# Optimization experiments

Measured on AMD Instinct MI355X. Metric: run time of the kernel, lower is better.

The kernel has to match this reference:

```python
import jax, jax.numpy as jnp
import numpy as np

NUM_CLASSES = 80
TOPK = 1000
CONF_THRESH = 0.05
NMS_THRESH = 0.6
IMG = 1280.0  # input image H = W
LEVEL_N = [230400, 57600, 14400, 3600, 900]  # (1280/stride)^2 * 9 anchors, strides 8..128


def _make_boxes(k, n):
    kc, kw = jax.random.split(k)
    cxcy = jax.random.uniform(kc, (n, 2), jnp.float32, 0.0, IMG)
    wh = jax.random.uniform(kw, (n, 2), jnp.float32, 8.0, 256.0)
    x1y1 = jnp.clip(cxcy - 0.5 * wh, 0.0, IMG)
    x2y2 = jnp.clip(cxcy + 0.5 * wh, 0.0, IMG)
    return jnp.concatenate([x1y1, x2y2], axis=-1)  # [n,4] xyxy pixel coords


def setup_inputs() -> dict:
    key = jax.random.key(0)
    keys = jax.random.split(key, 10)
    inp = {}
    for i, n in enumerate(LEVEL_N):
        inp[f"cls{i}"] = jax.random.normal(keys[i], (n, NUM_CLASSES), jnp.float32) - 2.0
        inp[f"box{i}"] = _make_boxes(keys[5 + i], n)
    return inp


def _level_topk(cls_l, box_l):
    # cls_l: [N, C] logits, box_l: [N, 4]
    n = cls_l.shape[0]
    scores = jax.nn.sigmoid(cls_l).reshape(-1)           # [N*C]
    k = min(TOPK, n)
    top_scores, top_idx = jax.lax.top_k(scores, k)       # fused sort/topk per level
    labels = top_idx % NUM_CLASSES
    anchor = top_idx // NUM_CLASSES
    boxes = box_l[anchor]                                # irregular gather
    valid = top_scores > CONF_THRESH
    return top_scores, labels, boxes, valid


def _pairwise_iou(b):
    # b: [M,4] xyxy
    area = jnp.maximum(b[:, 2] - b[:, 0], 0.0) * jnp.maximum(b[:, 3] - b[:, 1], 0.0)
    lt = jnp.maximum(b[:, None, :2], b[None, :, :2])
    rb = jnp.minimum(b[:, None, 2:], b[None, :, 2:])
    wh = jnp.maximum(rb - lt, 0.0)
    inter = wh[..., 0] * wh[..., 1]
    return inter / (area[:, None] + area[None, :] - inter + 1e-9)


def _greedy_nms(boxes, scores, labels, valid):
    # class-aware greedy NMS via per-class coordinate offset trick
    m = scores.shape[0]
    s = jnp.where(valid, scores, 0.0)
    order = jnp.argsort(-s)
    boxes = boxes[order]
    s = s[order]
    labels = labels[order]
    valid = valid[order]
    offset = labels.astype(boxes.dtype)[:, None] * (IMG + 1.0)
    ious = _pairwise_iou(boxes + offset)                 # [M,M]
    idx = jnp.arange(m)

    def body(i, keep):
        sup = keep[i] & (ious[i] > NMS_THRESH) & (idx > i)
        return keep & ~sup

    keep = jax.lax.fori_loop(0, m, body, valid)
    return boxes, s, labels, keep


def reference(cls0, cls1, cls2, cls3, cls4, box0, box1, box2, box3, box4):
    cls_preds = [cls0, cls1, cls2, cls3, cls4]
    box_preds = [box0, box1, box2, box3, box4]
    parts = [_level_topk(c, b) for c, b in zip(cls_preds, box_preds)]
    scores = jnp.concatenate([p[0] for p in parts])
    labels = jnp.concatenate([p[1] for p in parts])
    boxes = jnp.concatenate([p[2] for p in parts])
    valid = jnp.concatenate([p[3] for p in parts])
    boxes, scores, labels, keep = _greedy_nms(boxes, scores, labels, valid)
    keepf = keep.astype(boxes.dtype)
    bboxes = jnp.clip(boxes / IMG, 0.0, 1.0) * keepf[:, None]  # normalize like inference_single_image
    scores = scores * keepf
    return bboxes, scores, labels, keep
```

## Files before the change

### kernel.cpp

```cpp
#include <hip/hip_runtime.h>
#include <cmath>

typedef unsigned int u32;
typedef unsigned long long u64;

#define NLEV 5
#define M_TOT 4900
#define NWORDS 77
#define CSTRIDE 80
#define PAD_M 4928
#define NBLK 2999
#define LDSQ 2048
#define NSH 32
#define SHCAP 2048
#define OVCAP 16384
#define NREG 33
#define LVST (NSH*SHCAP + OVCAP)
#define TIE_CAP 4096
#define NBLK_CMAT 3003
#define HBINS 4096
#define UCAP 128

__constant__ int   c_KLVL[5] = {1000,1000,1000,1000,900};
__constant__ int   c_LOFF[5] = {0,1000,2000,3000,4000};
__constant__ int   c_N4[5]   = {4608000,1152000,288000,72000,18000};
__constant__ int   c_BB[6]   = {0,2250,2813,2954,2990,2999};
__constant__ float c_THR[5]  = {1.0f,0.65f,0.30f,-0.15f,-0.60f};

constexpr size_t OFF_CNT   = 0;
constexpr size_t OFF_OCNT  = 768;
constexpr size_t OFF_KEPT  = 1024;
constexpr size_t OFF_HPRED = 2048;
constexpr size_t OFF_C0    = 2816;
constexpr size_t OFF_KK    = 2848;
constexpr size_t OFF_EMITC = 2880;
constexpr size_t OFF_TIEC  = 2912;
constexpr size_t OFF_GHIST = 4096;
constexpr size_t ZERO_BYTES= OFF_GHIST + (size_t)NLEV*HBINS*4;
constexpr size_t OFF_TIEB  = ZERO_BYTES;
constexpr size_t OFF_CAND  = OFF_TIEB + (size_t)NLEV*TIE_CAP*8;
constexpr size_t OFF_KEY   = OFF_CAND + (size_t)NLEV*LVST*8;
constexpr size_t OFF_RAWB  = OFF_KEY   + (size_t)PAD_M*8;
constexpr size_t OFF_OFFB  = OFF_RAWB  + (size_t)PAD_M*16;
constexpr size_t OFF_LAB   = OFF_OFFB  + (size_t)PAD_M*16;
constexpr size_t OFF_SVAL  = OFF_LAB   + (size_t)PAD_M*4;
constexpr size_t OFF_VALID = OFF_SVAL  + (size_t)PAD_M*4;
constexpr size_t OFF_SRAWB = OFF_VALID + (size_t)PAD_M*4;
constexpr size_t OFF_SOFFB = OFF_SRAWB + (size_t)PAD_M*16;
constexpr size_t OFF_SLAB  = OFF_SOFFB + (size_t)PAD_M*16;
constexpr size_t OFF_SSVAL = OFF_SLAB  + (size_t)PAD_M*4;
constexpr size_t OFF_SVALID= OFF_SSVAL + (size_t)PAD_M*4;
constexpr size_t OFF_CMAT  = (OFF_SVALID + (size_t)PAD_M*4 + 255) & ~(size_t)255;

__device__ __forceinline__ u32 okey(u32 u){
  return (u & 0x80000000u) ? ~u : (u | 0x80000000u);
}

__device__ __forceinline__ u32 qbin(u32 bits, float T){
  float x = __uint_as_float(bits);
  int b = (int)((x - T)*800.0f);
  return (u32)max(0, min(HBINS-1, b));
}

__device__ __forceinline__ u32 lane_prior(u64 mask){
  return __builtin_amdgcn_mbcnt_hi((u32)(mask>>32),
         __builtin_amdgcn_mbcnt_lo((u32)mask, 0u));
}

__device__ __forceinline__ u32 wave_alloc(u32* ctr, bool take){
  u64 mask = __ballot(take);
  if (mask==0ull) return 0xFFFFFFFFu;
  u32 prior = lane_prior(mask);
  u32 total = (u32)__popcll(mask);
  int leader = __ffsll((unsigned long long)mask) - 1;
  u32 base = 0;
  if (take && prior==0u) base = atomicAdd(ctr, total);
  base = __shfl(base, leader, 64);
  return take ? (base + prior) : 0xFFFFFFFFu;
}

__device__ __forceinline__ const u32* region_ptr(u32* cand, int l, int r){
  return cand + ((size_t)l*LVST + ((r<NSH)?(size_t)r*SHCAP:(size_t)NSH*SHCAP))*2u;
}

__global__ void __launch_bounds__(256)
k_collect(const float* __restrict__ a0, const float* __restrict__ a1,
          const float* __restrict__ a2, const float* __restrict__ a3,
          const float* __restrict__ a4,
          u32* __restrict__ cnt, u32* __restrict__ ocnt, u32* __restrict__ cand)
{
  const int b = blockIdx.x;
  const int l = (b<c_BB[1])?0:(b<c_BB[2])?1:(b<c_BB[3])?2:(b<c_BB[4])?3:4;
  const float* __restrict__ p = (l==0)?a0:(l==1)?a1:(l==2)?a2:(l==3)?a3:a4;
  const float T = c_THR[l];
  const int n4l = c_N4[l];
  const int lb  = b - c_BB[l];
  const int shard = lb & (NSH-1);
  const int base4 = lb*2048 + (int)threadIdx.x;

  __shared__ u32 lcnt, gbase;
  __shared__ u32 lbitsA[LDSQ];
  __shared__ u32 lidxA[LDSQ];
  if (threadIdx.x==0) lcnt=0u;
  __syncthreads();

  float4 xs[8];
#pragma unroll
  for (int u=0;u<8;u++){
    int q = base4 + u*256;
    int qc = (q < n4l) ? q : (n4l-1);
    xs[u] = *(const float4*)(p + (size_t)qc*4u);
  }
  u32* cdS = cand + ((size_t)l*LVST + (size_t)shard*SHCAP)*2u;
  u32* cdO = cand + ((size_t)l*LVST + (size_t)NSH*SHCAP)*2u;
#pragma unroll
  for (int u=0;u<8;u++){
    int q = base4 + u*256;
    if (q < n4l){
      float v[4]={xs[u].x,xs[u].y,xs[u].z,xs[u].w};
#pragma unroll
      for (int i=0;i<4;i++){
        if (v[i] > T){
          u32 s = atomicAdd(&lcnt,1u);
          u32 bits = __float_as_uint(v[i]);
          u32 idx  = (u32)(q*4+i);
          if (s < LDSQ){ lbitsA[s]=bits; lidxA[s]=idx; }
          else {
            u32 pp = atomicAdd(&ocnt[l],1u);
            if (pp < OVCAP){ u32* d=cdO+(size_t)pp*2u; d[0]=bits; d[1]=idx; }
          }
        }
      }
    }
  }
  __syncthreads();
  if (threadIdx.x==0){
    u32 m = min(lcnt,(u32)LDSQ);
    gbase = (m>0u) ? atomicAdd(&cnt[l*NSH+shard],m) : 0xFFFFFFFFu;
  }
  __syncthreads();
  u32 m = min(lcnt,(u32)LDSQ);
  for (u32 i=threadIdx.x;i<m;i+=256u){
    u32 pp = gbase + i;
    if (pp < SHCAP){ u32* d=cdS+(size_t)pp*2u; d[0]=lbitsA[i]; d[1]=lidxA[i]; }
    else {
      u32 q = atomicAdd(&ocnt[l],1u);
      if (q < OVCAP){ u32* d=cdO+(size_t)q*2u; d[0]=lbitsA[i]; d[1]=lidxA[i]; }
    }
  }
}

__global__ void __launch_bounds__(256)
k_hist(const u32* __restrict__ cnt, const u32* __restrict__ ocnt,
       u32* __restrict__ cand, u32* __restrict__ ghist)
{
  const int l = blockIdx.x / NREG;
  const int r = blockIdx.x % NREG;
  const u32 len = (r<NSH) ? min(cnt[l*NSH+r],(u32)SHCAP) : min(ocnt[l],(u32)OVCAP);
  __shared__ u32 lh[HBINS];
  for (u32 i=threadIdx.x;i<(u32)HBINS;i+=256u) lh[i]=0u;
  __syncthreads();
  if (len){
    const u32* cdR = region_ptr(cand,l,r);
    const float Tl = c_THR[l];
    for (u32 i=threadIdx.x;i<len;i+=256u)
      atomicAdd(&lh[qbin(cdR[2*(size_t)i],Tl)],1u);
  }
  __syncthreads();
  u32* gh = ghist + (u32)l*HBINS;
  for (u32 i=threadIdx.x;i<(u32)HBINS;i+=256u){
    u32 v=lh[i];
    if (v) atomicAdd(&gh[i],v);
  }
}

__global__ void __launch_bounds__(1024)
k_cut(u32* __restrict__ cnt, u32* __restrict__ ocnt, u32* __restrict__ cand,
      u32* __restrict__ ghist,
      const float* __restrict__ a0, const float* __restrict__ a1,
      const float* __restrict__ a2, const float* __restrict__ a3,
      const float* __restrict__ a4,
      u32* __restrict__ c0A, u32* __restrict__ kkA)
{
  const int l = blockIdx.x;
  const int k = c_KLVL[l];
  const float Tl = c_THR[l];
  const float* __restrict__ p = (l==0)?a0:(l==1)?a1:(l==2)?a2:(l==3)?a3:a4;
  u32* cdO = cand + ((size_t)l*LVST + (size_t)NSH*SHCAP)*2u;
  u32* gh = ghist + (u32)l*HBINS;

  __shared__ u32 rlen[NREG];
  __shared__ u32 count_s, sufw[16];
  __shared__ u32 c0_s, kk_s;
  const u32 tid=threadIdx.x, lane=tid&63u, wave=tid>>6;
  if (tid<NSH) rlen[tid]=min(cnt[l*NSH+tid],(u32)SHCAP);
  if (tid==NSH) rlen[NSH]=min(ocnt[l],(u32)OVCAP);
  if (tid==0){ c0_s=0u; kk_s=(u32)k; }
  __syncthreads();
  if (tid==0){ u32 c=0; for(int r=0;r<NREG;r++) c+=rlen[r]; count_s=c; }
  __syncthreads();
  u32 count = count_s;

  if (count < (u32)k){
    const int nElem = c_N4[l]*4;
    float Tprev = Tl;
    u32 oc0 = rlen[NSH];
    for (int r=1; r<=7 && count<(u32)k; r++){
      float Tn = (r<7) ? (Tl - 1.5f*(float)r) : -3.0e38f;
      for (u32 i=tid; i<(u32)nElem; i+=1024u){
        float x = p[i];
        if (x>Tn && x<=Tprev){
          u32 pp = atomicAdd(&ocnt[l],1u);
          if (pp<OVCAP){ u32* d=cdO+(size_t)pp*2u; d[0]=__float_as_uint(x); d[1]=i; }
        }
      }
      __syncthreads();
      if (tid==0){
        rlen[NSH]=min(atomicAdd(&ocnt[l],0u),(u32)OVCAP);
        u32 c=0; for(int rr=0;rr<NREG;rr++) c+=rlen[rr]; count_s=c;
      }
      __syncthreads();
      count = count_s;
      Tprev = Tn;
    }
    if (tid==0 && rlen[NSH]>oc0) atomicAdd(&gh[0], rlen[NSH]-oc0);
    __syncthreads();
  }

  if (count > (u32)k){
    u32 base = tid*4u;
    u32 hb[4]; u32 ls=0u;
#pragma unroll
    for (int b2_=0;b2_<4;b2_++){ u32 h=gh[base+(u32)b2_]; hb[b2_]=h; ls+=h; }
    u32 x = ls;
#pragma unroll
    for (int off=1; off<64; off<<=1){
      u32 y = __shfl_down(x, off, 64);
      if (lane + (u32)off < 64u) x += y;
    }
    if (lane==0u) sufw[wave]=x;
    __syncthreads();
    u32 wsuf=0u;
    for (u32 w=wave+1u;w<16u;w++) wsuf += sufw[w];
    u32 suffix_after = wsuf + (x - ls);
    if (suffix_after < (u32)k && (u32)k <= suffix_after + ls){
      u32 run = suffix_after;
      for (int b2_=3;b2_>=0;b2_--){
        u32 h = hb[b2_];
        run += h;
        if (run >= (u32)k){ c0_s = base+(u32)b2_; kk_s = (u32)k - (run - h); break; }
      }
    }
    __syncthreads();
  }
  if (tid==0){ c0A[l]=c0_s; kkA[l]=kk_s; }
}

__device__ __forceinline__ void emit_record(int l, int slot, u32 lbits, u32 idx,
    const float4* __restrict__ boxp, u64* keyA, float4* rawbA, float4* offbA,
    u32* labA, float* svalA, u32* validA)
{
#pragma clang fp contract(off)
  float x = __uint_as_float(lbits);
  float s = (float)(1.0 / (1.0 + exp(-(double)x)));
  u32 valid = (s > 0.05f) ? 1u : 0u;
  u32 label = idx % 80u;
  u32 anchor = idx / 80u;
  float4 bx = boxp[anchor];
  float off = (float)label * 1281.0f;
  float4 ob;
  ob.x = bx.x + off; ob.y = bx.y + off; ob.z = bx.z + off; ob.w = bx.w + off;
  u32 pos = ((u32)l << 25) | idx;
  u32 khi = valid ? okey(lbits) : 0u;
  int g = c_LOFF[l] + slot;
  keyA[g]  = ((u64)khi << 32) | (u64)(u32)(~pos);
  rawbA[g] = bx; offbA[g] = ob; labA[g] = label;
  svalA[g] = valid ? s : 0.0f; validA[g] = valid;
}

__device__ __forceinline__ void emit_dummy(int l, int slot,
    u64* keyA, float4* rawbA, float4* offbA, u32* labA, float* svalA, u32* validA)
{
  u32 pos = ((u32)l<<25) | (0x1FFFFFFu - (u32)slot);
  int g = c_LOFF[l]+slot;
  float4 z; z.x=z.y=z.z=z.w=0.0f;
  keyA[g]=(u64)(u32)(~pos);
  rawbA[g]=z; offbA[g]=z; labA[g]=0u; svalA[g]=0.0f; validA[g]=0u;
}

__global__ void __launch_bounds__(256)
k_emit(const u32* __restrict__ cnt, const u32* __restrict__ ocnt,
       u32* __restrict__ cand,
       const u32* __restrict__ c0A,
       u32* __restrict__ emitc, u32* __restrict__ tiec, u32* __restrict__ tieb,
       const float4* b0, const float4* b1, const float4* b2,
       const float4* b3, const float4* b4,
       u64* keyA, float4* rawbA, float4* offbA,
       u32* labA, float* svalA, u32* validA)
{
  const int l = blockIdx.x / NREG;
  const int r = blockIdx.x % NREG;
  const u32 len = (r<NSH) ? min(cnt[l*NSH+r],(u32)SHCAP) : min(ocnt[l],(u32)OVCAP);
  if (len==0u) return;
  const float4* boxp = (l==0)?b0:(l==1)?b1:(l==2)?b2:(l==3)?b3:b4;
  const u32* cdR = region_ptr(cand,l,r);
  const float Tl = c_THR[l];
  const u32 c0 = c0A[l];
  const int k = c_KLVL[l];
  u32* tbL = tieb + (size_t)l*TIE_CAP*2u;

  __shared__ u32 wb[1024], wi[1024], tb2[1024], ti2[1024];
  __shared__ u32 nw_s, nt_s, gb_s, tgb_s;
  const u32 tid=threadIdx.x;
  if (tid==0){ nw_s=0u; nt_s=0u; }
  __syncthreads();

  u32 iters=(len+255u)/256u;
  for (u32 it=0; it<iters; it++){
    u32 i = it*256u + tid;
    bool in = i < len;
    u32 bits = in ? cdR[2*(size_t)i] : 0u;
    u32 idx  = in ? cdR[2*(size_t)i+1] : 0u;
    u32 h    = in ? qbin(bits,Tl) : 0u;
    bool hi  = in && (h > c0);
    bool tie = in && (h == c0);
    u32 s = wave_alloc(&nw_s, hi);
    if (hi && s<1024u){ wb[s]=bits; wi[s]=idx; }
    u32 t = wave_alloc(&nt_s, tie);
    if (tie){
      if (t<1024u){ tb2[t]=bits; ti2[t]=idx; }
      else {
        u32 g=atomicAdd(&tiec[l],1u);
        if (g<(u32)TIE_CAP){ tbL[2u*g]=bits; tbL[2u*g+1u]=idx; }
      }
    }
  }
  __syncthreads();
  u32 nw = min(nw_s,1024u), nt = min(nt_s,1024u);
  if (tid==0){
    gb_s  = nw ? atomicAdd(&emitc[l], nw) : 0u;
    tgb_s = nt ? atomicAdd(&tiec[l], nt) : 0u;
  }
  __syncthreads();
  for (u32 i=tid;i<nw;i+=256u){
    u32 slot = gb_s + i;
    if ((int)slot < k)
      emit_record(l,(int)slot,wb[i],wi[i],boxp,keyA,rawbA,offbA,labA,svalA,validA);
  }
  for (u32 i=tid;i<nt;i+=256u){
    u32 g = tgb_s + i;
    if (g<(u32)TIE_CAP){ tbL[2u*g]=tb2[i]; tbL[2u*g+1u]=ti2[i]; }
  }
}

__global__ void __launch_bounds__(1024)
k_tie(const u32* __restrict__ cnt, const u32* __restrict__ ocnt,
      u32* __restrict__ cand,
      const u32* __restrict__ c0A, const u32* __restrict__ kkA,
      u32* __restrict__ emitc, const u32* __restrict__ tiec,
      const u32* __restrict__ tieb,
      const float4* b0, const float4* b1, const float4* b2,
      const float4* b3, const float4* b4,
      u64* keyA, float4* rawbA, float4* offbA,
      u32* labA, float* svalA, u32* validA)
{
  const int l = blockIdx.x;
  const float4* boxp = (l==0)?b0:(l==1)?b1:(l==2)?b2:(l==3)?b3:b4;
  const int k = c_KLVL[l];
  const u32 kk = kkA[l];
  const u32 c0 = c0A[l];
  const float Tl = c_THR[l];
  const u32* tbL = tieb + (size_t)l*TIE_CAP*2u;
  const u32 ntg = tiec[l];
  const u32 tid = threadIdx.x;

  __shared__ u32 tb[TIE_CAP], ti[TIE_CAP];

  if (ntg <= (u32)TIE_CAP){
    for (u32 i=tid;i<ntg;i+=1024u){ tb[i]=tbL[2u*i]; ti[i]=tbL[2u*i+1u]; }
    __syncthreads();
    for (u32 e=tid;e<ntg;e+=1024u){
      u32 mk = okey(tb[e]); u32 mi = ti[e];
      u32 r=0u;
      for (u32 e2=0;e2<ntg;e2++){
        u32 k2 = okey(tb[e2]);
        r += (k2>mk || (k2==mk && ti[e2]<mi)) ? 1u : 0u;
      }
      if (r < kk){
        u32 s = atomicAdd(&emitc[l],1u);
        if ((int)s < k)
          emit_record(l,(int)s,tb[e],mi,boxp,keyA,rawbA,offbA,labA,svalA,validA);
      }
    }
  } else {
    for (int r0=0;r0<NREG;r0++){
      const u32* cdR = region_ptr(cand,l,r0);
      u32 len = (r0<NSH)?min(cnt[l*NSH+r0],(u32)SHCAP):min(ocnt[l],(u32)OVCAP);
      for (u32 i=tid;i<len;i+=1024u){
        u32 bits=cdR[2*(size_t)i], idx=cdR[2*(size_t)i+1];
        if (qbin(bits,Tl)!=c0) continue;
        u32 mk=okey(bits); u32 rank=0u;
        for (int r2=0;r2<NREG;r2++){
          const u32* c2 = region_ptr(cand,l,r2);
          u32 len2 = (r2<NSH)?min(cnt[l*NSH+r2],(u32)SHCAP):min(ocnt[l],(u32)OVCAP);
          for (u32 j=0;j<len2;j++){
            u32 b2=c2[2*(size_t)j];
            if (qbin(b2,Tl)!=c0) continue;
            u32 k2=okey(b2);
            rank += (k2>mk || (k2==mk && c2[2*(size_t)j+1]<idx)) ? 1u : 0u;
          }
        }
        if (rank<kk){
          u32 s=atomicAdd(&emitc[l],1u);
          if ((int)s<k)
            emit_record(l,(int)s,bits,idx,boxp,keyA,rawbA,offbA,labA,svalA,validA);
        }
      }
    }
  }
  __syncthreads();
  __shared__ u32 em_s;
  if (tid==0) em_s = atomicAdd(&emitc[l],0u);
  __syncthreads();
  u32 em = min(em_s,(u32)k);
  for (u32 i=em+tid;i<(u32)k;i+=1024u)
    emit_dummy(l,(int)i,keyA,rawbA,offbA,labA,svalA,validA);
}

__global__ void __launch_bounds__(256)
k_rank(const u64* __restrict__ keyA,
       const float4* __restrict__ rawbA, const float4* __restrict__ offbA,
       const u32* __restrict__ labA, const float* __restrict__ svalA,
       const u32* __restrict__ validA,
       float4* srawb, float4* soffb, u32* slab, float* ssval, u32* svalid)
{
  __shared__ u64 sk[M_TOT];
  __shared__ u32 part[3][64];
  for (int i=threadIdx.x;i<M_TOT;i+=256) sk[i]=keyA[i];
  __syncthreads();
  int lane = threadIdx.x & 63;
  int wave = threadIdx.x >> 6;
  int i = blockIdx.x*64 + lane;
  u64 mk = sk[(i<M_TOT)?i:0];
  int j0 = wave*1225;
  u32 r=0;
#pragma unroll 5
  for (int j=j0;j<j0+1225;j++) r += (sk[j]>mk)?1u:0u;
  if (wave) part[wave-1][lane]=r;
  __syncthreads();
  if (wave==0 && i<M_TOT){
    r += part[0][lane]+part[1][lane]+part[2][lane];
    srawb[r]=rawbA[i]; soffb[r]=offbA[i]; slab[r]=labA[i];
    ssval[r]=svalA[i]; svalid[r]=validA[i];
  }
}

__global__ void __launch_bounds__(256)
k_cmat(const float4* __restrict__ soffb, u64* __restrict__ cmat,
       u64* __restrict__ haspred)
{
#pragma clang fp contract(off)
  int bi = blockIdx.x;
  int jt = (int)((sqrtf(8.0f*(float)bi+1.0f)-1.0f)*0.5f);
  while ((jt+1)*(jt+2)/2 <= bi) jt++;
  while (jt*(jt+1)/2 > bi) jt--;
  int wt = bi - jt*(jt+1)/2;

  __shared__ float rx[64],ry[64],rz[64],rw[64],ra[64];
  __shared__ float cx[64],cy[64],cz[64],cw[64],cae[64];
  int tid = threadIdx.x;
  if (tid<64){
    float4 b = soffb[wt*64+tid];
    rx[tid]=b.x; ry[tid]=b.y; rz[tid]=b.z; rw[tid]=b.w;
    ra[tid]=fmaxf(b.z-b.x,0.0f)*fmaxf(b.w-b.y,0.0f);
  } else if (tid<128){
    int c=tid-64;
    float4 b = soffb[jt*64+c];
    cx[c]=b.x; cy[c]=b.y; cz[c]=b.z; cw[c]=b.w;
    cae[c]=fmaxf(b.z-b.x,0.0f)*fmaxf(b.w-b.y,0.0f);
  }
  __syncthreads();
  int lane = tid & 63;
  int wave = tid >> 6;
  int rowg = wt*64 + lane;
  float bx=rx[lane], by=ry[lane], bz=rz[lane], bw=rw[lane], bar=ra[lane];
  for (int cc=wave*16; cc<wave*16+16; cc++){
    int jg = jt*64 + cc;
    if (jg >= M_TOT) continue;
    float jx=cx[cc], jy=cy[cc], jz=cz[cc], jw=cw[cc], jar=cae[cc];
    float ltx=fmaxf(bx,jx), lty=fmaxf(by,jy);
    float rbx=fminf(bz,jz), rby=fminf(bw,jw);
    float wx=fmaxf(rbx-ltx,0.0f), wy=fmaxf(rby-lty,0.0f);
    float inter=wx*wy;
    float iou = inter/(bar+jar-inter+1e-9f);
    bool bit = (rowg < jg) && (iou > 0.6f);
    u64 word = __ballot(bit);
    if (lane==0){
      cmat[(size_t)jg*CSTRIDE + (size_t)wt] = word;
      if (word) atomicOr(&haspred[jg>>6], 1ull<<(jg&63));
    }
  }
}

__global__ void __launch_bounds__(256)
k_resolve(const u64* __restrict__ cmat, const u32* __restrict__ svalid,
          const u64* __restrict__ haspred, u64* __restrict__ kept)
{
  __shared__ u64 k0[NWORDS];
  __shared__ u64 uw[NWORDS];
  __shared__ u32 ubase[NWORDS];
  __shared__ unsigned short ulist[UCAP];
  __shared__ u64 pmask[UCAP][2];
  __shared__ u32 dhit[UCAP];
  __shared__ u32 nu_s;
  const u32 tid=threadIdx.x, lane=tid&63u, wave=tid>>6;

  for (u32 w=wave; w<NWORDS; w+=4){
    int j = (int)(w*64u+lane);
    u32 sv = (j<M_TOT)? svalid[j] : 0u;
    u64 hp = haspred[w];
    bool hpb = (hp>>lane)&1ull;
    u64 keepb = __ballot(sv && !hpb);
    u64 undb  = __ballot(sv && hpb);
    if (lane==0){ k0[w]=keepb; uw[w]=undb; }
  }
  __syncthreads();
  if (tid==0){
    u32 n=0;
    for (int w=0;w<NWORDS;w++){
      ubase[w]=n;
      u64 U=uw[w];
      while(U){ int b=__builtin_ctzll(U); U&=U-1ull;
                if (n<UCAP) ulist[n]=(unsigned short)(w*64+b); n++; }
    }
    nu_s=n;
  }
  __syncthreads();
  u32 nu = nu_s;

  if (nu>0u && nu<=UCAP){
    for (u32 t=tid; t<nu; t+=256u){
      u32 j = (u32)ulist[t];
      const u64* row = cmat + (size_t)j*CSTRIDE;
      u32 wmax = j>>6;
      u64 hit=0ull, pm0=0ull, pm1=0ull;
      for (u32 w=0; w<=wmax; w++){
        u64 rw = row[w];
        hit |= rw & k0[w];
        u64 ub = rw & uw[w];
        while(ub){
          int b=__builtin_ctzll(ub); ub&=ub-1ull;
          u32 idx = ubase[w] + (u32)__popcll(uw[w] & ((b==0)?0ull:((1ull<<b)-1ull)));
          if (idx<64u) pm0 |= 1ull<<idx; else pm1 |= 1ull<<(idx-64u);
        }
      }
      dhit[t] = (hit!=0ull)?1u:0u;
      pmask[t][0]=pm0; pmask[t][1]=pm1;
    }
    __syncthreads();
    if (tid==0){
      u64 ku0=0ull, ku1=0ull;
      for (u32 t=0;t<nu;t++){
        bool sup = dhit[t] || ((pmask[t][0]&ku0)|(pmask[t][1]&ku1))!=0ull;
        if (!sup){
          if (t<64u) ku0|=1ull<<t; else ku1|=1ull<<(t-64u);
          u32 j=(u32)ulist[t];
          k0[j>>6] |= 1ull<<(j&63u);
        }
      }
    }
    __syncthreads();
  } else if (nu>UCAP){
    if (tid==0){
      for (int w=0;w<NWORDS;w++){
        u64 U=uw[w];
        while(U){
          int b=__builtin_ctzll(U); U&=U-1ull;
          u32 j=(u32)(w*64+b);
          const u64* row = cmat + (size_t)j*CSTRIDE;
          u64 hit=0ull; u32 wmax=j>>6;
          for (u32 w2=0;w2<=wmax;w2++) hit |= row[w2] & k0[w2];
          if (hit==0ull) k0[j>>6] |= 1ull<<(j&63u);
        }
      }
    }
    __syncthreads();
  }
  for (u32 w=tid; w<NWORDS; w+=256u) kept[w]=k0[w];
}

__global__ void k_out(const u64* __restrict__ kept, const float4* __restrict__ srawb,
                      const float* __restrict__ ssval, const u32* __restrict__ slab,
                      float* __restrict__ out)
{
  int t=blockIdx.x*blockDim.x+threadIdx.x;
  if (t<M_TOT){
    u32 kb=(u32)((kept[t>>6]>>(t&63))&1ull);
    float kf=kb?1.0f:0.0f;
    float4 b=srawb[t];
    out[4*t+0]=fminf(fmaxf(b.x/1280.0f,0.0f),1.0f)*kf;
    out[4*t+1]=fminf(fmaxf(b.y/1280.0f,0.0f),1.0f)*kf;
    out[4*t+2]=fminf(fmaxf(b.z/1280.0f,0.0f),1.0f)*kf;
    out[4*t+3]=fminf(fmaxf(b.w/1280.0f,0.0f),1.0f)*kf;
    out[19600+t]=ssval[t]*kf;
    out[24500+t]=(float)slab[t];
    out[29400+t]=kf;
  }
}

extern "C" void kernel_launch(void* const* d_in, const int* in_sizes, int n_in,
                              void* d_out, int out_size, void* d_ws, size_t ws_size,
                              hipStream_t stream)
{
  const float* cls[5]={nullptr,nullptr,nullptr,nullptr,nullptr};
  const float* box[5]={nullptr,nullptr,nullptr,nullptr,nullptr};
  static const int clsEl[5]={18432000,4608000,1152000,288000,72000};
  static const int boxEl[5]={921600,230400,57600,14400,3600};
  for (int i=0;i<n_in;i++){
    int sz=in_sizes[i];
    bool done=false;
    for (int l=0;l<5 && !done;l++){
      if (sz==clsEl[l] && !cls[l]){ cls[l]=(const float*)d_in[i]; done=true; }
      else if (sz==boxEl[l] && !box[l]){ box[l]=(const float*)d_in[i]; done=true; }
    }
  }
  unsigned char* ws=(unsigned char*)d_ws;
  u32* cnt   = (u32*)(ws+OFF_CNT);
  u32* ocnt  = (u32*)(ws+OFF_OCNT);
  u64* kept  = (u64*)(ws+OFF_KEPT);
  u64* hpred = (u64*)(ws+OFF_HPRED);
  u32* c0A   = (u32*)(ws+OFF_C0);
  u32* kkA   = (u32*)(ws+OFF_KK);
  u32* emitc = (u32*)(ws+OFF_EMITC);
  u32* tiec  = (u32*)(ws+OFF_TIEC);
  u32* ghist = (u32*)(ws+OFF_GHIST);
  u32* tieb  = (u32*)(ws+OFF_TIEB);
  u32* cand  = (u32*)(ws+OFF_CAND);
  u64* keyA  = (u64*)(ws+OFF_KEY);
  float4* rawbA=(float4*)(ws+OFF_RAWB);
  float4* offbA=(float4*)(ws+OFF_OFFB);
  u32* labA  = (u32*)(ws+OFF_LAB);
  float* svalA=(float*)(ws+OFF_SVAL);
  u32* validA=(u32*)(ws+OFF_VALID);
  float4* srawb=(float4*)(ws+OFF_SRAWB);
  float4* soffb=(float4*)(ws+OFF_SOFFB);
  u32* slab  = (u32*)(ws+OFF_SLAB);
  float* ssval=(float*)(ws+OFF_SSVAL);
  u32* svalid=(u32*)(ws+OFF_SVALID);
  u64* cmat  = (u64*)(ws+OFF_CMAT);
  float* out = (float*)d_out;

  hipMemsetAsync(ws, 0, ZERO_BYTES, stream);

  k_collect<<<dim3(NBLK),dim3(256),0,stream>>>(cls[0],cls[1],cls[2],cls[3],cls[4],cnt,ocnt,cand);
  k_hist   <<<dim3(NLEV*NREG),dim3(256),0,stream>>>(cnt,ocnt,cand,ghist);
  k_cut    <<<dim3(NLEV),dim3(1024),0,stream>>>(cnt,ocnt,cand,ghist,
              cls[0],cls[1],cls[2],cls[3],cls[4],c0A,kkA);
  k_emit   <<<dim3(NLEV*NREG),dim3(256),0,stream>>>(cnt,ocnt,cand,c0A,emitc,tiec,tieb,
              (const float4*)box[0],(const float4*)box[1],(const float4*)box[2],
              (const float4*)box[3],(const float4*)box[4],
              keyA,rawbA,offbA,labA,svalA,validA);
  k_tie    <<<dim3(NLEV),dim3(1024),0,stream>>>(cnt,ocnt,cand,c0A,kkA,emitc,tiec,tieb,
              (const float4*)box[0],(const float4*)box[1],(const float4*)box[2],
              (const float4*)box[3],(const float4*)box[4],
              keyA,rawbA,offbA,labA,svalA,validA);
  k_rank   <<<dim3(77),dim3(256),0,stream>>>(keyA,rawbA,offbA,labA,svalA,validA,
                                             srawb,soffb,slab,ssval,svalid);
  k_cmat   <<<dim3(NBLK_CMAT),dim3(256),0,stream>>>(soffb,cmat,hpred);
  k_resolve<<<dim3(1),dim3(256),0,stream>>>(cmat,svalid,hpred,kept);
  k_out    <<<dim3(20),dim3(256),0,stream>>>(kept,srawb,ssval,slab,out);
}
```

Before: 238.7 us.

## Fuse post-collect stages into one persistent kernel with grid barriers

Replaces the eight launches that follow collection (hist, cut, emit, tie, rank, cmat, resolve, out) with a single 256-block persistent kernel. The stages are separated by software grid-wide barriers built on an atomic counter, and each stage's shared memory is reused through a union. This removes per-launch overhead and inter-kernel gaps. In exchange, stages that used 1024-thread blocks now run on 256 threads, the cmat stage presumably loops over its roughly 3000 tiles on 256 blocks, and the barrier only works if all 256 blocks are resident at the same time.

```diff
diff --git a/kernel.cpp b/kernel.cpp
--- a/kernel.cpp
+++ b/kernel.cpp
@@ -20,6 +20,7 @@
 #define NBLK_CMAT 3003
 #define HBINS 4096
 #define UCAP 128
+#define MEGA_BLKS 256
 
 __constant__ int   c_KLVL[5] = {1000,1000,1000,1000,900};
 __constant__ int   c_LOFF[5] = {0,1000,2000,3000,4000};
@@ -35,6 +36,7 @@
 constexpr size_t OFF_KK    = 2848;
 constexpr size_t OFF_EMITC = 2880;
 constexpr size_t OFF_TIEC  = 2912;
+constexpr size_t OFF_BAR   = 2944;
 constexpr size_t OFF_GHIST = 4096;
 constexpr size_t ZERO_BYTES= OFF_GHIST + (size_t)NLEV*HBINS*4;
 constexpr size_t OFF_TIEB  = ZERO_BYTES;
@@ -148,112 +150,6 @@
       if (q < OVCAP){ u32* d=cdO+(size_t)q*2u; d[0]=lbitsA[i]; d[1]=lidxA[i]; }
     }
   }
-}
-
-__global__ void __launch_bounds__(256)
-k_hist(const u32* __restrict__ cnt, const u32* __restrict__ ocnt,
-       u32* __restrict__ cand, u32* __restrict__ ghist)
-{
-  const int l = blockIdx.x / NREG;
-  const int r = blockIdx.x % NREG;
-  const u32 len = (r<NSH) ? min(cnt[l*NSH+r],(u32)SHCAP) : min(ocnt[l],(u32)OVCAP);
-  __shared__ u32 lh[HBINS];
-  for (u32 i=threadIdx.x;i<(u32)HBINS;i+=256u) lh[i]=0u;
-  __syncthreads();
-  if (len){
-    const u32* cdR = region_ptr(cand,l,r);
-    const float Tl = c_THR[l];
-    for (u32 i=threadIdx.x;i<len;i+=256u)
-      atomicAdd(&lh[qbin(cdR[2*(size_t)i],Tl)],1u);
-  }
-  __syncthreads();
-  u32* gh = ghist + (u32)l*HBINS;
-  for (u32 i=threadIdx.x;i<(u32)HBINS;i+=256u){
-    u32 v=lh[i];
-    if (v) atomicAdd(&gh[i],v);
-  }
-}
-
-__global__ void __launch_bounds__(1024)
-k_cut(u32* __restrict__ cnt, u32* __restrict__ ocnt, u32* __restrict__ cand,
-      u32* __restrict__ ghist,
-      const float* __restrict__ a0, const float* __restrict__ a1,
-      const float* __restrict__ a2, const float* __restrict__ a3,
-      const float* __restrict__ a4,
-      u32* __restrict__ c0A, u32* __restrict__ kkA)
-{
-  const int l = blockIdx.x;
-  const int k = c_KLVL[l];
-  const float Tl = c_THR[l];
-  const float* __restrict__ p = (l==0)?a0:(l==1)?a1:(l==2)?a2:(l==3)?a3:a4;
-  u32* cdO = cand + ((size_t)l*LVST + (size_t)NSH*SHCAP)*2u;
-  u32* gh = ghist + (u32)l*HBINS;
-
-  __shared__ u32 rlen[NREG];
-  __shared__ u32 count_s, sufw[16];
-  __shared__ u32 c0_s, kk_s;
-  const u32 tid=threadIdx.x, lane=tid&63u, wave=tid>>6;
-  if (tid<NSH) rlen[tid]=min(cnt[l*NSH+tid],(u32)SHCAP);
-  if (tid==NSH) rlen[NSH]=min(ocnt[l],(u32)OVCAP);
-  if (tid==0){ c0_s=0u; kk_s=(u32)k; }
-  __syncthreads();
-  if (tid==0){ u32 c=0; for(int r=0;r<NREG;r++) c+=rlen[r]; count_s=c; }
-  __syncthreads();
-  u32 count = count_s;
-
-  if (count < (u32)k){
-    const int nElem = c_N4[l]*4;
-    float Tprev = Tl;
-    u32 oc0 = rlen[NSH];
-    for (int r=1; r<=7 && count<(u32)k; r++){
-      float Tn = (r<7) ? (Tl - 1.5f*(float)r) : -3.0e38f;
-      for (u32 i=tid; i<(u32)nElem; i+=1024u){
-        float x = p[i];
-        if (x>Tn && x<=Tprev){
-          u32 pp = atomicAdd(&ocnt[l],1u);
-          if (pp<OVCAP){ u32* d=cdO+(size_t)pp*2u; d[0]=__float_as_uint(x); d[1]=i; }
-        }
-      }
-      __syncthreads();
-      if (tid==0){
-        rlen[NSH]=min(atomicAdd(&ocnt[l],0u),(u32)OVCAP);
-        u32 c=0; for(int rr=0;rr<NREG;rr++) c+=rlen[rr]; count_s=c;
-      }
-      __syncthreads();
-      count = count_s;
-      Tprev = Tn;
-    }
-    if (tid==0 && rlen[NSH]>oc0) atomicAdd(&gh[0], rlen[NSH]-oc0);
-    __syncthreads();
-  }
-
-  if (count > (u32)k){
-    u32 base = tid*4u;
-    u32 hb[4]; u32 ls=0u;
-#pragma unroll
-    for (int b2_=0;b2_<4;b2_++){ u32 h=gh[base+(u32)b2_]; hb[b2_]=h; ls+=h; }
-    u32 x = ls;
-#pragma unroll
-    for (int off=1; off<64; off<<=1){
-      u32 y = __shfl_down(x, off, 64);
-      if (lane + (u32)off < 64u) x += y;
-    }
-    if (lane==0u) sufw[wave]=x;
-    __syncthreads();
-    u32 wsuf=0u;
-    for (u32 w=wave+1u;w<16u;w++) wsuf += sufw[w];
-    u32 suffix_after = wsuf + (x - ls);
-    if (suffix_after < (u32)k && (u32)k <= suffix_after + ls){
-      u32 run = suffix_after;
-      for (int b2_=3;b2_>=0;b2_--){
-        u32 h = hb[b2_];
-        run += h;
-        if (run >= (u32)k){ c0_s = base+(u32)b2_; kk_s = (u32)k - (run - h); break; }
-      }
-    }
-    __syncthreads();
-  }
-  if (tid==0){ c0A[l]=c0_s; kkA[l]=kk_s; }
 }
 
 __device__ __forceinline__ void emit_record(int l, int slot, u32 lbits, u32 idx,
@@ -288,323 +184,410 @@
   rawbA[g]=z; offbA[g]=z; labA[g]=0u; svalA[g]=0.0f; validA[g]=0u;
 }
 
+struct SmHist { u32 lh[HBINS]; };
+struct SmCut  { u32 rlen[NREG]; u32 sufw[4]; u32 count_s, c0_s, kk_s; };
+struct SmEmit { u32 wb[1024], wi[1024], tb2[1024], ti2[1024]; u32 nw, nt, gb, tgb; };
+struct SmTie  { u32 tb[TIE_CAP], ti[TIE_CAP]; u32 em; };
+struct SmRank { u64 sk[M_TOT]; u32 part[3][64]; };
+struct SmCmat { float rx[64],ry[64],rz[64],rw[64],ra[64];
+                float cx[64],cy[64],cz[64],cw[64],cae[64]; };
+struct SmRes  { u64 k0[NWORDS], uw[NWORDS]; u64 pmask[UCAP][2]; u32 ubase[NWORDS];
+                unsigned short ulist[UCAP]; u32 dhit[UCAP]; u32 nu; };
+union SmAll { SmHist h; SmCut c; SmEmit e; SmTie t; SmRank r; SmCmat m; SmRes s; };
+
+struct MegaP {
+  u32 *cnt, *ocnt, *cand, *ghist, *bar;
+  const float *a0,*a1,*a2,*a3,*a4;
+  const float4 *b0,*b1,*b2,*b3,*b4;
+  u32 *c0A,*kkA,*emitc,*tiec,*tieb;
+  u64 *keyA; float4 *rawbA,*offbA; u32 *labA; float *svalA; u32 *validA;
+  float4 *srawb,*soffb; u32 *slab; float *ssval; u32 *svalid;
+  u64 *cmat,*hpred,*kept; float* out;
+};
+
+__device__ __forceinline__ void gsync(u32* bar, u32 target){
+  __syncthreads();
+  __threadfence();
+  if (threadIdx.x==0){
+    atomicAdd(bar, 1u);
+    while (atomicAdd(bar, 0u) < target) __builtin_amdgcn_s_sleep(2);
+  }
+  __syncthreads();
+  __threadfence();
+}
+
 __global__ void __launch_bounds__(256)
-k_emit(const u32* __restrict__ cnt, const u32* __restrict__ ocnt,
-       u32* __restrict__ cand,
-       const u32* __restrict__ c0A,
-       u32* __restrict__ emitc, u32* __restrict__ tiec, u32* __restrict__ tieb,
-       const float4* b0, const float4* b1, const float4* b2,
-       const float4* b3, const float4* b4,
-       u64* keyA, float4* rawbA, float4* offbA,
-       u32* labA, float* svalA, u32* validA)
+k_mega(MegaP P)
 {
-  const int l = blockIdx.x / NREG;
-  const int r = blockIdx.x % NREG;
-  const u32 len = (r<NSH) ? min(cnt[l*NSH+r],(u32)SHCAP) : min(ocnt[l],(u32)OVCAP);
-  if (len==0u) return;
-  const float4* boxp = (l==0)?b0:(l==1)?b1:(l==2)?b2:(l==3)?b3:b4;
-  const u32* cdR = region_ptr(cand,l,r);
-  const float Tl = c_THR[l];
-  const u32 c0 = c0A[l];
-  const int k = c_KLVL[l];
-  u32* tbL = tieb + (size_t)l*TIE_CAP*2u;
-
-  __shared__ u32 wb[1024], wi[1024], tb2[1024], ti2[1024];
-  __shared__ u32 nw_s, nt_s, gb_s, tgb_s;
-  const u32 tid=threadIdx.x;
-  if (tid==0){ nw_s=0u; nt_s=0u; }
-  __syncthreads();
-
-  u32 iters=(len+255u)/256u;
-  for (u32 it=0; it<iters; it++){
-    u32 i = it*256u + tid;
-    bool in = i < len;
-    u32 bits = in ? cdR[2*(size_t)i] : 0u;
-    u32 idx  = in ? cdR[2*(size_t)i+1] : 0u;
-    u32 h    = in ? qbin(bits,Tl) : 0u;
-    bool hi  = in && (h > c0);
-    bool tie = in && (h == c0);
-    u32 s = wave_alloc(&nw_s, hi);
-    if (hi && s<1024u){ wb[s]=bits; wi[s]=idx; }
-    u32 t = wave_alloc(&nt_s, tie);
-    if (tie){
-      if (t<1024u){ tb2[t]=bits; ti2[t]=idx; }
-      else {
-        u32 g=atomicAdd(&tiec[l],1u);
-        if (g<(u32)TIE_CAP){ tbL[2u*g]=bits; tbL[2u*g+1u]=idx; }
-      }
-    }
-  }
-  __syncthreads();
-  u32 nw = min(nw_s,1024u), nt = min(nt_s,1024u);
-  if (tid==0){
-    gb_s  = nw ? atomicAdd(&emitc[l], nw) : 0u;
-    tgb_s = nt ? atomicAdd(&tiec[l], nt) : 0u;
-  }
-  __syncthreads();
-  for (u32 i=tid;i<nw;i+=256u){
-    u32 slot = gb_s + i;
-    if ((int)slot < k)
-      emit_record(l,(int)slot,wb[i],wi[i],boxp,keyA,rawbA,offbA,labA,svalA,validA);
-  }
-  for (u32 i=tid;i<nt;i+=256u){
-    u32 g = tgb_s + i;
-    if (g<(u32)TIE_CAP){ tbL[2u*g]=tb2[i]; tbL[2u*g+1u]=ti2[i]; }
-  }
-}
-
-__global__ void __launch_bounds__(1024)
-k_tie(const u32* __restrict__ cnt, const u32* __restrict__ ocnt,
-      u32* __restrict__ cand,
-      const u32* __restrict__ c0A, const u32* __restrict__ kkA,
-      u32* __restrict__ emitc, const u32* __restrict__ tiec,
-      const u32* __restrict__ tieb,
-      const float4* b0, const float4* b1, const float4* b2,
-      const float4* b3, const float4* b4,
-      u64* keyA, float4* rawbA, float4* offbA,
-      u32* labA, float* svalA, u32* validA)
-{
-  const int l = blockIdx.x;
-  const float4* boxp = (l==0)?b0:(l==1)?b1:(l==2)?b2:(l==3)?b3:b4;
-  const int k = c_KLVL[l];
-  const u32 kk = kkA[l];
-  const u32 c0 = c0A[l];
-  const float Tl = c_THR[l];
-  const u32* tbL = tieb + (size_t)l*TIE_CAP*2u;
-  const u32 ntg = tiec[l];
+  __shared__ SmAll sm;
   const u32 tid = threadIdx.x;
-
-  __shared__ u32 tb[TIE_CAP], ti[TIE_CAP];
-
-  if (ntg <= (u32)TIE_CAP){
-    for (u32 i=tid;i<ntg;i+=1024u){ tb[i]=tbL[2u*i]; ti[i]=tbL[2u*i+1u]; }
-    __syncthreads();
-    for (u32 e=tid;e<ntg;e+=1024u){
-      u32 mk = okey(tb[e]); u32 mi = ti[e];
-      u32 r=0u;
-      for (u32 e2=0;e2<ntg;e2++){
-        u32 k2 = okey(tb[e2]);
-        r += (k2>mk || (k2==mk && ti[e2]<mi)) ? 1u : 0u;
-      }
-      if (r < kk){
-        u32 s = atomicAdd(&emitc[l],1u);
-        if ((int)s < k)
-          emit_record(l,(int)s,tb[e],mi,boxp,keyA,rawbA,offbA,labA,svalA,validA);
-      }
-    }
-  } else {
-    for (int r0=0;r0<NREG;r0++){
-      const u32* cdR = region_ptr(cand,l,r0);
-      u32 len = (r0<NSH)?min(cnt[l*NSH+r0],(u32)SHCAP):min(ocnt[l],(u32)OVCAP);
-      for (u32 i=tid;i<len;i+=1024u){
-        u32 bits=cdR[2*(size_t)i], idx=cdR[2*(size_t)i+1];
-        if (qbin(bits,Tl)!=c0) continue;
-        u32 mk=okey(bits); u32 rank=0u;
-        for (int r2=0;r2<NREG;r2++){
-          const u32* c2 = region_ptr(cand,l,r2);
-          u32 len2 = (r2<NSH)?min(cnt[l*NSH+r2],(u32)SHCAP):min(ocnt[l],(u32)OVCAP);
-          for (u32 j=0;j<len2;j++){
-            u32 b2=c2[2*(size_t)j];
-            if (qbin(b2,Tl)!=c0) continue;
-            u32 k2=okey(b2);
-            rank += (k2>mk || (k2==mk && c2[2*(size_t)j+1]<idx)) ? 1u : 0u;
-          }
-        }
-        if (rank<kk){
-          u32 s=atomicAdd(&emitc[l],1u);
-          if ((int)s<k)
-            emit_record(l,(int)s,bits,idx,boxp,keyA,rawbA,offbA,labA,svalA,validA);
-        }
-      }
-    }
-  }
-  __syncthreads();
-  __shared__ u32 em_s;
-  if (tid==0) em_s = atomicAdd(&emitc[l],0u);
-  __syncthreads();
-  u32 em = min(em_s,(u32)k);
-  for (u32 i=em+tid;i<(u32)k;i+=1024u)
-    emit_dummy(l,(int)i,keyA,rawbA,offbA,labA,svalA,validA);
-}
-
-__global__ void __launch_bounds__(256)
-k_rank(const u64* __restrict__ keyA,
-       const float4* __restrict__ rawbA, const float4* __restrict__ offbA,
-       const u32* __restrict__ labA, const float* __restrict__ svalA,
-       const u32* __restrict__ validA,
-       float4* srawb, float4* soffb, u32* slab, float* ssval, u32* svalid)
-{
-  __shared__ u64 sk[M_TOT];
-  __shared__ u32 part[3][64];
-  for (int i=threadIdx.x;i<M_TOT;i+=256) sk[i]=keyA[i];
-  __syncthreads();
-  int lane = threadIdx.x & 63;
-  int wave = threadIdx.x >> 6;
-  int i = blockIdx.x*64 + lane;
-  u64 mk = sk[(i<M_TOT)?i:0];
-  int j0 = wave*1225;
-  u32 r=0;
+  const u32 lane = tid & 63u;
+  const u32 wave = tid >> 6;
+
+  if (blockIdx.x < (u32)(NLEV*NREG)){
+    const int l = (int)blockIdx.x / NREG;
+    const int r = (int)blockIdx.x % NREG;
+    const u32 len = (r<NSH) ? min(P.cnt[l*NSH+r],(u32)SHCAP) : min(P.ocnt[l],(u32)OVCAP);
+    for (u32 i=tid;i<(u32)HBINS;i+=256u) sm.h.lh[i]=0u;
+    __syncthreads();
+    if (len){
+      const u32* cdR = region_ptr(P.cand,l,r);
+      const float Tl = c_THR[l];
+      for (u32 i=tid;i<len;i+=256u)
+        atomicAdd(&sm.h.lh[qbin(cdR[2*(size_t)i],Tl)],1u);
+    }
+    __syncthreads();
+    u32* gh = P.ghist + (u32)l*HBINS;
+    for (u32 i=tid;i<(u32)HBINS;i+=256u){
+      u32 v=sm.h.lh[i];
+      if (v) atomicAdd(&gh[i],v);
+    }
+  }
+  gsync(P.bar, 1u*MEGA_BLKS);
+
+  if (blockIdx.x < (u32)NLEV){
+    const int l = (int)blockIdx.x;
+    const int k = c_KLVL[l];
+    const float Tl = c_THR[l];
+    const float* p = (l==0)?P.a0:(l==1)?P.a1:(l==2)?P.a2:(l==3)?P.a3:P.a4;
+    u32* cdO = P.cand + ((size_t)l*LVST + (size_t)NSH*SHCAP)*2u;
+    u32* gh = P.ghist + (u32)l*HBINS;
+
+    if (tid<NSH) sm.c.rlen[tid]=min(P.cnt[l*NSH+tid],(u32)SHCAP);
+    if (tid==NSH) sm.c.rlen[NSH]=min(P.ocnt[l],(u32)OVCAP);
+    if (tid==0){ sm.c.c0_s=0u; sm.c.kk_s=(u32)k; }
+    __syncthreads();
+    if (tid==0){ u32 c=0; for(int r=0;r<NREG;r++) c+=sm.c.rlen[r]; sm.c.count_s=c; }
+    __syncthreads();
+    u32 count = sm.c.count_s;
+
+    if (count < (u32)k){
+      const int nElem = c_N4[l]*4;
+      float Tprev = Tl;
+      u32 oc0 = sm.c.rlen[NSH];
+      for (int r=1; r<=7 && count<(u32)k; r++){
+        float Tn = (r<7) ? (Tl - 1.5f*(float)r) : -3.0e38f;
+        for (u32 i=tid; i<(u32)nElem; i+=256u){
+          float x = p[i];
+          if (x>Tn && x<=Tprev){
+            u32 pp = atomicAdd(&P.ocnt[l],1u);
+            if (pp<OVCAP){ u32* d=cdO+(size_t)pp*2u; d[0]=__float_as_uint(x); d[1]=i; }
+          }
+        }
+        __syncthreads();
+        if (tid==0){
+          sm.c.rlen[NSH]=min(atomicAdd(&P.ocnt[l],0u),(u32)OVCAP);
+          u32 c=0; for(int rr=0;rr<NREG;rr++) c+=sm.c.rlen[rr]; sm.c.count_s=c;
+        }
+        __syncthreads();
+        count = sm.c.count_s;
+        Tprev = Tn;
+      }
+      if (tid==0 && sm.c.rlen[NSH]>oc0) atomicAdd(&gh[0], sm.c.rlen[NSH]-oc0);
+      __syncthreads();
+    }
+
+    if (count > (u32)k){
+      u32 base = tid*16u;
+      u32 hb[16]; u32 ls=0u;
+#pragma unroll
+      for (int b2_=0;b2_<16;b2_++){ u32 h=gh[base+(u32)b2_]; hb[b2_]=h; ls+=h; }
+      u32 x = ls;
+#pragma unroll
+      for (int off=1; off<64; off<<=1){
+        u32 y = __shfl_down(x, off, 64);
+        if (lane + (u32)off < 64u) x += y;
+      }
+      if (lane==0u) sm.c.sufw[wave]=x;
+      __syncthreads();
+      u32 wsuf=0u;
+      for (u32 w=wave+1u;w<4u;w++) wsuf += sm.c.sufw[w];
+      u32 suffix_after = wsuf + (x - ls);
+      if (suffix_after < (u32)k && (u32)k <= suffix_after + ls){
+        u32 run = suffix_after;
+        for (int b2_=15;b2_>=0;b2_--){
+          u32 h = hb[b2_];
+          run += h;
+          if (run >= (u32)k){ sm.c.c0_s = base+(u32)b2_; sm.c.kk_s = (u32)k - (run - h); break; }
+        }
+      }
+      __syncthreads();
+    }
+    if (tid==0){ P.c0A[l]=sm.c.c0_s; P.kkA[l]=sm.c.kk_s; }
+  }
+  gsync(P.bar, 2u*MEGA_BLKS);
+
+  if (blockIdx.x < (u32)(NLEV*NREG)){
+    const int l = (int)blockIdx.x / NREG;
+    const int r = (int)blockIdx.x % NREG;
+    const u32 len = (r<NSH) ? min(P.cnt[l*NSH+r],(u32)SHCAP) : min(P.ocnt[l],(u32)OVCAP);
+    if (len){
+      const float4* boxp = (l==0)?P.b0:(l==1)?P.b1:(l==2)?P.b2:(l==3)?P.b3:P.b4;
+      const u32* cdR = region_ptr(P.cand,l,r);
+      const float Tl = c_THR[l];
+      const u32 c0 = P.c0A[l];
+      const int k = c_KLVL[l];
+      u32* tbL = P.tieb + (size_t)l*TIE_CAP*2u;
+
+      if (tid==0){ sm.e.nw=0u; sm.e.nt=0u; }
+      __syncthreads();
+      u32 iters=(len+255u)/256u;
+      for (u32 it=0; it<iters; it++){
+        u32 i = it*256u + tid;
+        bool in = i < len;
+        u32 bits = in ? cdR[2*(size_t)i] : 0u;
+        u32 idx  = in ? cdR[2*(size_t)i+1] : 0u;
+        u32 h    = in ? qbin(bits,Tl) : 0u;
+        bool hi  = in && (h > c0);
+        bool tie = in && (h == c0);
+        u32 s = wave_alloc(&sm.e.nw, hi);
+        if (hi && s<1024u){ sm.e.wb[s]=bits; sm.e.wi[s]=idx; }
+        u32 t = wave_alloc(&sm.e.nt, tie);
+        if (tie){
+          if (t<1024u){ sm.e.tb2[t]=bits; sm.e.ti2[t]=idx; }
+          else {
+            u32 g=atomicAdd(&P.tiec[l],1u);
+            if (g<(u32)TIE_CAP){ tbL[2u*g]=bits; tbL[2u*g+1u]=idx; }
+          }
+        }
+      }
+      __syncthreads();
+      u32 nw = min(sm.e.nw,1024u), nt = min(sm.e.nt,1024u);
+      if (tid==0){
+        sm.e.gb  = nw ? atomicAdd(&P.emitc[l], nw) : 0u;
+        sm.e.tgb = nt ? atomicAdd(&P.tiec[l], nt) : 0u;
+      }
+      __syncthreads();
+      for (u32 i=tid;i<nw;i+=256u){
+        u32 slot = sm.e.gb + i;
+        if ((int)slot < k)
+          emit_record(l,(int)slot,sm.e.wb[i],sm.e.wi[i],boxp,
+                      P.keyA,P.rawbA,P.offbA,P.labA,P.svalA,P.validA);
+      }
+      for (u32 i=tid;i<nt;i+=256u){
+        u32 g = sm.e.tgb + i;
+        if (g<(u32)TIE_CAP){ tbL[2u*g]=sm.e.tb2[i]; tbL[2u*g+1u]=sm.e.ti2[i]; }
+      }
+    }
+  }
+  gsync(P.bar, 3u*MEGA_BLKS);
+
+  if (blockIdx.x < (u32)NLEV){
+    const int l = (int)blockIdx.x;
+    const float4* boxp = (l==0)?P.b0:(l==1)?P.b1:(l==2)?P.b2:(l==3)?P.b3:P.b4;
+    const int k = c_KLVL[l];
+    const u32 kk = P.kkA[l];
+    const u32 c0 = P.c0A[l];
+    const float Tl = c_THR[l];
+    const u32* tbL = P.tieb + (size_t)l*TIE_CAP*2u;
+    const u32 ntg = P.tiec[l];
+
+    if (ntg <= (u32)TIE_CAP){
+      for (u32 i=tid;i<ntg;i+=256u){ sm.t.tb[i]=tbL[2u*i]; sm.t.ti[i]=tbL[2u*i+1u]; }
+      __syncthreads();
+      for (u32 e=tid;e<ntg;e+=256u){
+        u32 mk = okey(sm.t.tb[e]); u32 mi = sm.t.ti[e];
+        u32 r=0u;
+        for (u32 e2=0;e2<ntg;e2++){
+          u32 k2 = okey(sm.t.tb[e2]);
+          r += (k2>mk || (k2==mk && sm.t.ti[e2]<mi)) ? 1u : 0u;
+        }
+        if (r < kk){
+          u32 s = atomicAdd(&P.emitc[l],1u);
+          if ((int)s < k)
+            emit_record(l,(int)s,sm.t.tb[e],mi,boxp,
+                        P.keyA,P.rawbA,P.offbA,P.labA,P.svalA,P.validA);
+        }
+      }
+    } else {
+      for (int r0=0;r0<NREG;r0++){
+        const u32* cdR = region_ptr(P.cand,l,r0);
+        u32 len = (r0<NSH)?min(P.cnt[l*NSH+r0],(u32)SHCAP):min(P.ocnt[l],(u32)OVCAP);
+        for (u32 i=tid;i<len;i+=256u){
+          u32 bits=cdR[2*(size_t)i], idx=cdR[2*(size_t)i+1];
+          if (qbin(bits,Tl)!=c0) continue;
+          u32 mk=okey(bits); u32 rank=0u;
+          for (int r2=0;r2<NREG;r2++){
+            const u32* c2 = region_ptr(P.cand,l,r2);
+            u32 len2 = (r2<NSH)?min(P.cnt[l*NSH+r2],(u32)SHCAP):min(P.ocnt[l],(u32)OVCAP);
+            for (u32 j=0;j<len2;j++){
+              u32 b2=c2[2*(size_t)j];
+              if (qbin(b2,Tl)!=c0) continue;
+              u32 k2=okey(b2);
+              rank += (k2>mk || (k2==mk && c2[2*(size_t)j+1]<idx)) ? 1u : 0u;
+            }
+          }
+          if (rank<kk){
+            u32 s=atomicAdd(&P.emitc[l],1u);
+            if ((int)s<k)
+              emit_record(l,(int)s,bits,idx,boxp,
+                          P.keyA,P.rawbA,P.offbA,P.labA,P.svalA,P.validA);
+          }
+        }
+      }
+    }
+    __syncthreads();
+    if (tid==0) sm.t.em = atomicAdd(&P.emitc[l],0u);
+    __syncthreads();
+    u32 em = min(sm.t.em,(u32)k);
+    for (u32 i=em+tid;i<(u32)k;i+=256u)
+      emit_dummy(l,(int)i,P.keyA,P.rawbA,P.offbA,P.labA,P.svalA,P.validA);
+  }
+  gsync(P.bar, 4u*MEGA_BLKS);
+
+  if (blockIdx.x < 77u){
+    for (int i=(int)tid;i<M_TOT;i+=256) sm.r.sk[i]=P.keyA[i];
+    __syncthreads();
+    int i = (int)blockIdx.x*64 + (int)lane;
+    u64 mk = sm.r.sk[(i<M_TOT)?i:0];
+    int j0 = (int)wave*1225;
+    u32 r=0;
 #pragma unroll 5
-  for (int j=j0;j<j0+1225;j++) r += (sk[j]>mk)?1u:0u;
-  if (wave) part[wave-1][lane]=r;
-  __syncthreads();
-  if (wave==0 && i<M_TOT){
-    r += part[0][lane]+part[1][lane]+part[2][lane];
-    srawb[r]=rawbA[i]; soffb[r]=offbA[i]; slab[r]=labA[i];
-    ssval[r]=svalA[i]; svalid[r]=validA[i];
-  }
-}
-
-__global__ void __launch_bounds__(256)
-k_cmat(const float4* __restrict__ soffb, u64* __restrict__ cmat,
-       u64* __restrict__ haspred)
-{
+    for (int j=j0;j<j0+1225;j++) r += (sm.r.sk[j]>mk)?1u:0u;
+    if (wave) sm.r.part[wave-1][lane]=r;
+    __syncthreads();
+    if (wave==0 && i<M_TOT){
+      r += sm.r.part[0][lane]+sm.r.part[1][lane]+sm.r.part[2][lane];
+      P.srawb[r]=P.rawbA[i]; P.soffb[r]=P.offbA[i]; P.slab[r]=P.labA[i];
+      P.ssval[r]=P.svalA[i]; P.svalid[r]=P.validA[i];
+    }
+  }
+  gsync(P.bar, 5u*MEGA_BLKS);
+
+  for (int bi=(int)blockIdx.x; bi<NBLK_CMAT; bi+=MEGA_BLKS){
 #pragma clang fp contract(off)
-  int bi = blockIdx.x;
-  int jt = (int)((sqrtf(8.0f*(float)bi+1.0f)-1.0f)*0.5f);
-  while ((jt+1)*(jt+2)/2 <= bi) jt++;
-  while (jt*(jt+1)/2 > bi) jt--;
-  int wt = bi - jt*(jt+1)/2;
-
-  __shared__ float rx[64],ry[64],rz[64],rw[64],ra[64];
-  __shared__ float cx[64],cy[64],cz[64],cw[64],cae[64];
-  int tid = threadIdx.x;
-  if (tid<64){
-    float4 b = soffb[wt*64+tid];
-    rx[tid]=b.x; ry[tid]=b.y; rz[tid]=b.z; rw[tid]=b.w;
-    ra[tid]=fmaxf(b.z-b.x,0.0f)*fmaxf(b.w-b.y,0.0f);
-  } else if (tid<128){
-    int c=tid-64;
-    float4 b = soffb[jt*64+c];
-    cx[c]=b.x; cy[c]=b.y; cz[c]=b.z; cw[c]=b.w;
-    cae[c]=fmaxf(b.z-b.x,0.0f)*fmaxf(b.w-b.y,0.0f);
-  }
-  __syncthreads();
-  int lane = tid & 63;
-  int wave = tid >> 6;
-  int rowg = wt*64 + lane;
-  float bx=rx[lane], by=ry[lane], bz=rz[lane], bw=rw[lane], bar=ra[lane];
-  for (int cc=wave*16; cc<wave*16+16; cc++){
-    int jg = jt*64 + cc;
-    if (jg >= M_TOT) continue;
-    float jx=cx[cc], jy=cy[cc], jz=cz[cc], jw=cw[cc], jar=cae[cc];
-    float ltx=fmaxf(bx,jx), lty=fmaxf(by,jy);
-    float rbx=fminf(bz,jz), rby=fminf(bw,jw);
-    float wx=fmaxf(rbx-ltx,0.0f), wy=fmaxf(rby-lty,0.0f);
-    float inter=wx*wy;
-    float iou = inter/(bar+jar-inter+1e-9f);
-    bool bit = (rowg < jg) && (iou > 0.6f);
-    u64 word = __ballot(bit);
-    if (lane==0){
-      cmat[(size_t)jg*CSTRIDE + (size_t)wt] = word;
-      if (word) atomicOr(&haspred[jg>>6], 1ull<<(jg&63));
-    }
-  }
-}
-
-__global__ void __launch_bounds__(256)
-k_resolve(const u64* __restrict__ cmat, const u32* __restrict__ svalid,
-          const u64* __restrict__ haspred, u64* __restrict__ kept)
-{
-  __shared__ u64 k0[NWORDS];
-  __shared__ u64 uw[NWORDS];
-  __shared__ u32 ubase[NWORDS];
-  __shared__ unsigned short ulist[UCAP];
-  __shared__ u64 pmask[UCAP][2];
-  __shared__ u32 dhit[UCAP];
-  __shared__ u32 nu_s;
-  const u32 tid=threadIdx.x, lane=tid&63u, wave=tid>>6;
-
-  for (u32 w=wave; w<NWORDS; w+=4){
-    int j = (int)(w*64u+lane);
-    u32 sv = (j<M_TOT)? svalid[j] : 0u;
-    u64 hp = haspred[w];
-    bool hpb = (hp>>lane)&1ull;
-    u64 keepb = __ballot(sv && !hpb);
-    u64 undb  = __ballot(sv && hpb);
-    if (lane==0){ k0[w]=keepb; uw[w]=undb; }
-  }
-  __syncthreads();
-  if (tid==0){
-    u32 n=0;
-    for (int w=0;w<NWORDS;w++){
-      ubase[w]=n;
-      u64 U=uw[w];
-      while(U){ int b=__builtin_ctzll(U); U&=U-1ull;
-                if (n<UCAP) ulist[n]=(unsigned short)(w*64+b); n++; }
-    }
-    nu_s=n;
-  }
-  __syncthreads();
-  u32 nu = nu_s;
-
-  if (nu>0u && nu<=UCAP){
-    for (u32 t=tid; t<nu; t+=256u){
-      u32 j = (u32)ulist[t];
-      const u64* row = cmat + (size_t)j*CSTRIDE;
-      u32 wmax = j>>6;
-      u64 hit=0ull, pm0=0ull, pm1=0ull;
-      for (u32 w=0; w<=wmax; w++){
-        u64 rw = row[w];
-        hit |= rw & k0[w];
-        u64 ub = rw & uw[w];
-        while(ub){
-          int b=__builtin_ctzll(ub); ub&=ub-1ull;
-          u32 idx = ubase[w] + (u32)__popcll(uw[w] & ((b==0)?0ull:((1ull<<b)-1ull)));
-          if (idx<64u) pm0 |= 1ull<<idx; else pm1 |= 1ull<<(idx-64u);
-        }
-      }
-      dhit[t] = (hit!=0ull)?1u:0u;
-      pmask[t][0]=pm0; pmask[t][1]=pm1;
+    int jt = (int)((sqrtf(8.0f*(float)bi+1.0f)-1.0f)*0.5f);
+    while ((jt+1)*(jt+2)/2 <= bi) jt++;
+    while (jt*(jt+1)/2 > bi) jt--;
+    int wt = bi - jt*(jt+1)/2;
+
+    if ((int)tid<64){
+      float4 b = P.soffb[wt*64+(int)tid];
+      sm.m.rx[tid]=b.x; sm.m.ry[tid]=b.y; sm.m.rz[tid]=b.z; sm.m.rw[tid]=b.w;
+      sm.m.ra[tid]=fmaxf(b.z-b.x,0.0f)*fmaxf(b.w-b.y,0.0f);
+    } else if ((int)tid<128){
+      int c=(int)tid-64;
+      float4 b = P.soffb[jt*64+c];
+      sm.m.cx[c]=b.x; sm.m.cy[c]=b.y; sm.m.cz[c]=b.z; sm.m.cw[c]=b.w;
+      sm.m.cae[c]=fmaxf(b.z-b.x,0.0f)*fmaxf(b.w-b.y,0.0f);
+    }
+    __syncthreads();
+    int rowg = wt*64 + (int)lane;
+    float bx=sm.m.rx[lane], by=sm.m.ry[lane], bz=sm.m.rz[lane],
+          bw=sm.m.rw[lane], bar2=sm.m.ra[lane];
+    for (int cc=(int)wave*16; cc<(int)wave*16+16; cc++){
+      int jg = jt*64 + cc;
+      if (jg >= M_TOT) continue;
+      float jx=sm.m.cx[cc], jy=sm.m.cy[cc], jz=sm.m.cz[cc],
+            jw=sm.m.cw[cc], jar=sm.m.cae[cc];
+      float ltx=fmaxf(bx,jx), lty=fmaxf(by,jy);
+      float rbx=fminf(bz,jz), rby=fminf(bw,jw);
+      float wx=fmaxf(rbx-ltx,0.0f), wy=fmaxf(rby-lty,0.0f);
+      float inter=wx*wy;
+      float iou = inter/(bar2+jar-inter+1e-9f);
+      bool bit = (rowg < jg) && (iou > 0.6f);
+      u64 word = __ballot(bit);
+      if (lane==0){
+        P.cmat[(size_t)jg*CSTRIDE + (size_t)wt] = word;
+        if (word) atomicOr(&P.hpred[jg>>6], 1ull<<(jg&63));
+      }
+    }
+    __syncthreads();
+  }
+  gsync(P.bar, 6u*MEGA_BLKS);
+
+  if (blockIdx.x==0u){
+    for (u32 w=wave; w<NWORDS; w+=4){
+      int j = (int)(w*64u+lane);
+      u32 sv = (j<M_TOT)? P.svalid[j] : 0u;
+      u64 hp = P.hpred[w];
+      bool hpb = (hp>>lane)&1ull;
+      u64 keepb = __ballot(sv && !hpb);
+      u64 undb  = __ballot(sv && hpb);
+      if (lane==0){ sm.s.k0[w]=keepb; sm.s.uw[w]=undb; }
     }
     __syncthreads();
     if (tid==0){
-      u64 ku0=0ull, ku1=0ull;
-      for (u32 t=0;t<nu;t++){
-        bool sup = dhit[t] || ((pmask[t][0]&ku0)|(pmask[t][1]&ku1))!=0ull;
-        if (!sup){
-          if (t<64u) ku0|=1ull<<t; else ku1|=1ull<<(t-64u);
-          u32 j=(u32)ulist[t];
-          k0[j>>6] |= 1ull<<(j&63u);
-        }
-      }
-    }
-    __syncthreads();
-  } else if (nu>UCAP){
-    if (tid==0){
+      u32 n=0;
       for (int w=0;w<NWORDS;w++){
-        u64 U=uw[w];
-        while(U){
-          int b=__builtin_ctzll(U); U&=U-1ull;
-          u32 j=(u32)(w*64+b);
-          const u64* row = cmat + (size_t)j*CSTRIDE;
-          u64 hit=0ull; u32 wmax=j>>6;
-          for (u32 w2=0;w2<=wmax;w2++) hit |= row[w2] & k0[w2];
-          if (hit==0ull) k0[j>>6] |= 1ull<<(j&63u);
-        }
-      }
-    }
-    __syncthreads();
-  }
-  for (u32 w=tid; w<NWORDS; w+=256u) kept[w]=k0[w];
-}
-
-__global__ void k_out(const u64* __restrict__ kept, const float4* __restrict__ srawb,
-                      const float* __restrict__ ssval, const u32* __restrict__ slab,
-                      float* __restrict__ out)
-{
-  int t=blockIdx.x*blockDim.x+threadIdx.x;
-  if (t<M_TOT){
-    u32 kb=(u32)((kept[t>>6]>>(t&63))&1ull);
-    float kf=kb?1.0f:0.0f;
-    float4 b=srawb[t];
-    out[4*t+0]=fminf(fmaxf(b.x/1280.0f,0.0f),1.0f)*kf;
-    out[4*t+1]=fminf(fmaxf(b.y/1280.0f,0.0f),1.0f)*kf;
-    out[4*t+2]=fminf(fmaxf(b.z/1280.0f,0.0f),1.0f)*kf;
-    out[4*t+3]=fminf(fmaxf(b.w/1280.0f,0.0f),1.0f)*kf;
-    out[19600+t]=ssval[t]*kf;
-    out[24500+t]=(float)slab[t];
-    out[29400+t]=kf;
+        sm.s.ubase[w]=n;
+        u64 U=sm.s.uw[w];
+        while(U){ int b=__builtin_ctzll(U); U&=U-1ull;
+                  if (n<UCAP) sm.s.ulist[n]=(unsigned short)(w*64+b); n++; }
+      }
+      sm.s.nu=n;
+    }
+    __syncthreads();
+    u32 nu = sm.s.nu;
+
+    if (nu>0u && nu<=UCAP){
+      for (u32 t=tid; t<nu; t+=256u){
+        u32 j = (u32)sm.s.ulist[t];
+        const u64* row = P.cmat + (size_t)j*CSTRIDE;
+        u32 wmax = j>>6;
+        u64 hit=0ull, pm0=0ull, pm1=0ull;
+        for (u32 w=0; w<=wmax; w++){
+          u64 rw = row[w];
+          hit |= rw & sm.s.k0[w];
+          u64 ub = rw & sm.s.uw[w];
+          while(ub){
+            int b=__builtin_ctzll(ub); ub&=ub-1ull;
+            u32 idx = sm.s.ubase[w] +
+                      (u32)__popcll(sm.s.uw[w] & ((b==0)?0ull:((1ull<<b)-1ull)));
+            if (idx<64u) pm0 |= 1ull<<idx; else pm1 |= 1ull<<(idx-64u);
+          }
+        }
+        sm.s.dhit[t] = (hit!=0ull)?1u:0u;
+        sm.s.pmask[t][0]=pm0; sm.s.pmask[t][1]=pm1;
+      }
+      __syncthreads();
+      if (tid==0){
+        u64 ku0=0ull, ku1=0ull;
+        for (u32 t=0;t<nu;t++){
+          bool sup = sm.s.dhit[t] ||
+                     ((sm.s.pmask[t][0]&ku0)|(sm.s.pmask[t][1]&ku1))!=0ull;
+          if (!sup){
+            if (t<64u) ku0|=1ull<<t; else ku1|=1ull<<(t-64u);
+            u32 j=(u32)sm.s.ulist[t];
+            sm.s.k0[j>>6] |= 1ull<<(j&63u);
+          }
+        }
+      }
+      __syncthreads();
+    } else if (nu>UCAP){
+      if (tid==0){
+        for (int w=0;w<NWORDS;w++){
+          u64 U=sm.s.uw[w];
+          while(U){
+            int b=__builtin_ctzll(U); U&=U-1ull;
+            u32 j=(u32)(w*64+b);
+            const u64* row = P.cmat + (size_t)j*CSTRIDE;
+            u64 hit=0ull; u32 wmax=j>>6;
+            for (u32 w2=0;w2<=wmax;w2++) hit |= row[w2] & sm.s.k0[w2];
+            if (hit==0ull) sm.s.k0[j>>6] |= 1ull<<(j&63u);
+          }
+        }
+      }
+      __syncthreads();
+    }
+    for (u32 w=tid; w<NWORDS; w+=256u) P.kept[w]=sm.s.k0[w];
+  }
+  gsync(P.bar, 7u*MEGA_BLKS);
+
+  {
+    int t=(int)blockIdx.x*256+(int)tid;
+    if (t<M_TOT){
+      u32 kb=(u32)((P.kept[t>>6]>>(t&63))&1ull);
+      float kf=kb?1.0f:0.0f;
+      float4 b=P.srawb[t];
+      P.out[4*t+0]=fminf(fmaxf(b.x/1280.0f,0.0f),1.0f)*kf;
+      P.out[4*t+1]=fminf(fmaxf(b.y/1280.0f,0.0f),1.0f)*kf;
+      P.out[4*t+2]=fminf(fmaxf(b.z/1280.0f,0.0f),1.0f)*kf;
+      P.out[4*t+3]=fminf(fmaxf(b.w/1280.0f,0.0f),1.0f)*kf;
+      P.out[19600+t]=P.ssval[t]*kf;
+      P.out[24500+t]=(float)P.slab[t];
+      P.out[29400+t]=kf;
+    }
   }
 }
 
@@ -625,48 +608,40 @@
     }
   }
   unsigned char* ws=(unsigned char*)d_ws;
-  u32* cnt   = (u32*)(ws+OFF_CNT);
-  u32* ocnt  = (u32*)(ws+OFF_OCNT);
-  u64* kept  = (u64*)(ws+OFF_KEPT);
-  u64* hpred = (u64*)(ws+OFF_HPRED);
-  u32* c0A   = (u32*)(ws+OFF_C0);
-  u32* kkA   = (u32*)(ws+OFF_KK);
-  u32* emitc = (u32*)(ws+OFF_EMITC);
-  u32* tiec  = (u32*)(ws+OFF_TIEC);
-  u32* ghist = (u32*)(ws+OFF_GHIST);
-  u32* tieb  = (u32*)(ws+OFF_TIEB);
-  u32* cand  = (u32*)(ws+OFF_CAND);
-  u64* keyA  = (u64*)(ws+OFF_KEY);
-  float4* rawbA=(float4*)(ws+OFF_RAWB);
-  float4* offbA=(float4*)(ws+OFF_OFFB);
-  u32* labA  = (u32*)(ws+OFF_LAB);
-  float* svalA=(float*)(ws+OFF_SVAL);
-  u32* validA=(u32*)(ws+OFF_VALID);
-  float4* srawb=(float4*)(ws+OFF_SRAWB);
-  float4* soffb=(float4*)(ws+OFF_SOFFB);
-  u32* slab  = (u32*)(ws+OFF_SLAB);
-  float* ssval=(float*)(ws+OFF_SSVAL);
-  u32* svalid=(u32*)(ws+OFF_SVALID);
-  u64* cmat  = (u64*)(ws+OFF_CMAT);
-  float* out = (float*)d_out;
+
+  MegaP P;
+  P.cnt   = (u32*)(ws+OFF_CNT);
+  P.ocnt  = (u32*)(ws+OFF_OCNT);
+  P.cand  = (u32*)(ws+OFF_CAND);
+  P.ghist = (u32*)(ws+OFF_GHIST);
+  P.bar   = (u32*)(ws+OFF_BAR);
+  P.a0=cls[0]; P.a1=cls[1]; P.a2=cls[2]; P.a3=cls[3]; P.a4=cls[4];
+  P.b0=(const float4*)box[0]; P.b1=(const float4*)box[1]; P.b2=(const float4*)box[2];
+  P.b3=(const float4*)box[3]; P.b4=(const float4*)box[4];
+  P.c0A  = (u32*)(ws+OFF_C0);
+  P.kkA  = (u32*)(ws+OFF_KK);
+  P.emitc= (u32*)(ws+OFF_EMITC);
+  P.tiec = (u32*)(ws+OFF_TIEC);
+  P.tieb = (u32*)(ws+OFF_TIEB);
+  P.keyA = (u64*)(ws+OFF_KEY);
+  P.rawbA=(float4*)(ws+OFF_RAWB);
+  P.offbA=(float4*)(ws+OFF_OFFB);
+  P.labA = (u32*)(ws+OFF_LAB);
+  P.svalA=(float*)(ws+OFF_SVAL);
+  P.validA=(u32*)(ws+OFF_VALID);
+  P.srawb=(float4*)(ws+OFF_SRAWB);
+  P.soffb=(float4*)(ws+OFF_SOFFB);
+  P.slab = (u32*)(ws+OFF_SLAB);
+  P.ssval=(float*)(ws+OFF_SSVAL);
+  P.svalid=(u32*)(ws+OFF_SVALID);
+  P.cmat = (u64*)(ws+OFF_CMAT);
+  P.hpred= (u64*)(ws+OFF_HPRED);
+  P.kept = (u64*)(ws+OFF_KEPT);
+  P.out  = (float*)d_out;
 
   hipMemsetAsync(ws, 0, ZERO_BYTES, stream);
 
-  k_collect<<<dim3(NBLK),dim3(256),0,stream>>>(cls[0],cls[1],cls[2],cls[3],cls[4],cnt,ocnt,cand);
-  k_hist   <<<dim3(NLEV*NREG),dim3(256),0,stream>>>(cnt,ocnt,cand,ghist);
-  k_cut    <<<dim3(NLEV),dim3(1024),0,stream>>>(cnt,ocnt,cand,ghist,
-              cls[0],cls[1],cls[2],cls[3],cls[4],c0A,kkA);
-  k_emit   <<<dim3(NLEV*NREG),dim3(256),0,stream>>>(cnt,ocnt,cand,c0A,emitc,tiec,tieb,
-              (const float4*)box[0],(const float4*)box[1],(const float4*)box[2],
-              (const float4*)box[3],(const float4*)box[4],
-              keyA,rawbA,offbA,labA,svalA,validA);
-  k_tie    <<<dim3(NLEV),dim3(1024),0,stream>>>(cnt,ocnt,cand,c0A,kkA,emitc,tiec,tieb,
-              (const float4*)box[0],(const float4*)box[1],(const float4*)box[2],
-              (const float4*)box[3],(const float4*)box[4],
-              keyA,rawbA,offbA,labA,svalA,validA);
-  k_rank   <<<dim3(77),dim3(256),0,stream>>>(keyA,rawbA,offbA,labA,svalA,validA,
-                                             srawb,soffb,slab,ssval,svalid);
-  k_cmat   <<<dim3(NBLK_CMAT),dim3(256),0,stream>>>(soffb,cmat,hpred);
-  k_resolve<<<dim3(1),dim3(256),0,stream>>>(cmat,svalid,hpred,kept);
-  k_out    <<<dim3(20),dim3(256),0,stream>>>(kept,srawb,ssval,slab,out);
-}
+  k_collect<<<dim3(NBLK),dim3(256),0,stream>>>(cls[0],cls[1],cls[2],cls[3],cls[4],
+                                               P.cnt,P.ocnt,(u32*)P.cand);
+  k_mega<<<dim3(MEGA_BLKS),dim3(256),0,stream>>>(P);
+}
```

New measurement: 524.0 us. +119.5%, slower.
